# Optimization experiments

Measured on AMD Instinct MI355X. Metric: run time of the kernel, lower is better.

The kernel has to match this reference:

```python
import jax, jax.numpy as jnp
import numpy as np

N = 6144
FEAT = 512
HID = 256
KMAX = 50
KNN = 20
SPATIAL_DECAY = 50.0
THR = 0.1


def setup_inputs() -> dict:
    key = jax.random.key(0)
    ks = jax.random.split(key, 4)
    features = jax.random.normal(ks[0], (N, FEAT), dtype=jnp.float32)
    # spatial coordinates in a ~1000um slide, matches spatial_decay=50
    positions = jax.random.uniform(ks[1], (N, 2), dtype=jnp.float32) * 1000.0
    W1 = jax.random.normal(ks[2], (FEAT, HID), dtype=jnp.float32) * np.float32(1.0 / np.sqrt(FEAT))
    b1 = jnp.zeros((HID,), jnp.float32)
    W2 = jax.random.normal(ks[3], (HID, KMAX), dtype=jnp.float32) * np.float32(1.0 / np.sqrt(HID))
    b2 = jnp.zeros((KMAX,), jnp.float32)
    return {
        "features": features,
        "positions": positions,
        "lambda_weight": jnp.asarray(0.5, jnp.float32),
        "temperature": jnp.asarray(1.0, jnp.float32),
        "spatial_weight": jnp.asarray(1.0, jnp.float32),
        "W1": W1, "b1": b1, "W2": W2, "b2": b2,
    }


def reference(features, positions, lambda_weight, temperature, spatial_weight, W1, b1, W2, b2):
    n = features.shape[0]
    # --- LearnableAdjacency (Eq. 6) ---
    norm = jnp.maximum(jnp.linalg.norm(features, axis=1, keepdims=True), 1e-12)
    fn = features / norm
    sim = fn @ fn.T                                  # [N,N]
    p2 = jnp.sum(positions * positions, axis=1)
    d2 = jnp.maximum(p2[:, None] + p2[None, :] - 2.0 * (positions @ positions.T), 0.0)
    spatial_k = jnp.exp(-d2 / (2.0 * SPATIAL_DECAY ** 2))
    lam = jax.nn.sigmoid(lambda_weight)
    adj = jax.nn.sigmoid((lam * sim + (1.0 - lam) * spatial_k) * temperature)
    # row-wise top-k mask (scatter of ones)
    _, topk_idx = jax.lax.top_k(adj, KNN)
    mask = jnp.zeros_like(adj).at[jnp.arange(n)[:, None], topk_idx].set(1.0)
    adj = adj * mask

    # --- edge_index <=> binary adjacency (threshold 0.1) ---
    A_bin = (adj > THR).astype(adj.dtype)            # edge pattern used by GCN + loss

    # --- DifferentiablePooling: 2-layer GCN over the edge pattern ---
    # PyG GCNConv: add self-loops (diag already 1 -> becomes 2), deg from target (col) sums,
    # edge norm d_r^{-1/2} d_c^{-1/2}, aggregate at target: out = Mn^T (X W) + b
    M = A_bin + jnp.eye(n, dtype=adj.dtype)
    dinv = jax.lax.rsqrt(jnp.sum(M, axis=0))
    Mn = (dinv[:, None] * M) * dinv[None, :]
    h = jax.nn.relu(Mn.T @ (features @ W1) + b1)
    s = Mn.T @ (h @ W2) + b2
    K = max(5, min(KMAX, int(np.ceil(N / 50))))      # static: 50
    S = jax.nn.softmax(s[:, :K], axis=1)             # [N,K]

    # --- spatial loss (Eq. 9), vectorized segment form ---
    # sum over edges (i,j): (S_i . S_j) * ||p_i - p_j||^2  == sum(S * ((A_bin*d2) @ S))
    E = jnp.sum(A_bin)
    We = A_bin * d2
    L_spatial = spatial_weight * jnp.sum(S * (We @ S)) / E

    # --- coarsening (Eq. 8) ---
    X_t = S.T @ features                             # [K,FEAT]
    A_coarse = S.T @ (adj @ S)                       # [K,K]
    A_t = A_coarse * (A_coarse > THR).astype(A_coarse.dtype)
    return (S, X_t, A_t, L_spatial, lam)
```

## Files before the change

### kernel.cpp

```cpp
#include <hip/hip_runtime.h>
#include <hip/hip_bf16.h>
#include <math.h>

#define N_PTS   6144
#define FEAT    512
#define HID     256
#define KMAX    50
#define KNN     20
#define THR     0.1f
#define CW      1536
#define NCHUNK  4

typedef unsigned short u16;
typedef __attribute__((ext_vector_type(8))) short bf16x8;
typedef __attribute__((ext_vector_type(8))) u16   u16x8;
typedef __attribute__((ext_vector_type(4))) float f32x4;

__device__ __forceinline__ u16 f2bf(float x) {
    union { float f; unsigned u; } a; a.f = x;
    unsigned r = (a.u + 0x7fffu + ((a.u >> 16) & 1u)) >> 16;
    return (u16)r;
}
__device__ __forceinline__ float bf2f(u16 h) {
    union { unsigned u; float f; } a; a.u = ((unsigned)h) << 16;
    return a.f;
}

__device__ __forceinline__ void gload16(const void* g, void* l) {
    __builtin_amdgcn_global_load_lds(
        (const __attribute__((address_space(1))) void*)g,
        (__attribute__((address_space(3))) void*)l, 16, 0, 0);
}

__global__ void init_kernel(int* __restrict__ indeg, int* __restrict__ fillc,
                            float* __restrict__ Ac, float* __restrict__ Xt,
                            int* __restrict__ ec) {
    int t = blockIdx.x * blockDim.x + threadIdx.x;
    if (t < N_PTS) { indeg[t] = 0; fillc[t] = 0; }
    if (t < KMAX * KMAX) Ac[t] = 0.f;
    if (t < KMAX * FEAT) Xt[t] = 0.f;
    if (t == 0) { ec[0] = 0; }
}

__global__ __launch_bounds__(64) void normalize_kernel(const float* __restrict__ f,
                                                       u16* __restrict__ fnh,
                                                       u16* __restrict__ fnl,
                                                       u16* __restrict__ fh_,
                                                       u16* __restrict__ fl_) {
    int row = blockIdx.x, lane = threadIdx.x;
    const float4* fr = (const float4*)(f + (size_t)row * FEAT);
    float4 v0 = fr[lane * 2 + 0];
    float4 v1 = fr[lane * 2 + 1];
    float ss = v0.x * v0.x + v0.y * v0.y + v0.z * v0.z + v0.w * v0.w
             + v1.x * v1.x + v1.y * v1.y + v1.z * v1.z + v1.w * v1.w;
#pragma unroll
    for (int m = 1; m < 64; m <<= 1) ss += __shfl_xor(ss, m);
    float nrm = fmaxf(sqrtf(ss), 1e-12f);
    float r[8] = { v0.x, v0.y, v0.z, v0.w, v1.x, v1.y, v1.z, v1.w };
    u16x8 h, l, rh, rl;
#pragma unroll
    for (int q = 0; q < 8; q++) {
        float vn = r[q] / nrm;
        u16 hb = f2bf(vn);
        h[q] = hb; l[q] = f2bf(vn - bf2f(hb));
        u16 rb = f2bf(r[q]);
        rh[q] = rb; rl[q] = f2bf(r[q] - bf2f(rb));
    }
    size_t base = (size_t)row * FEAT + lane * 8;
    *(u16x8*)(fnh + base) = h;
    *(u16x8*)(fnl + base) = l;
    *(u16x8*)(fh_ + base) = rh;
    *(u16x8*)(fl_ + base) = rl;
}

__global__ void p2_kernel(const float* __restrict__ pos, float* __restrict__ p2) {
    int i = blockIdx.x * blockDim.x + threadIdx.x;
    if (i < N_PTS) {
        float x = pos[2 * i], y = pos[2 * i + 1];
        p2[i] = x * x + y * y;
    }
}

__global__ __launch_bounds__(256) void w1t_split_kernel(const float* __restrict__ W1,
                                                        u16* __restrict__ th,
                                                        u16* __restrict__ tl) {
    int n = blockIdx.x;
    for (int k = threadIdx.x; k < FEAT; k += 256) {
        float v = W1[(size_t)k * HID + n];
        u16 hb = f2bf(v);
        th[(size_t)n * FEAT + k] = hb;
        tl[(size_t)n * FEAT + k] = f2bf(v - bf2f(hb));
    }
}

__global__ __launch_bounds__(256) void w2t_split_kernel(const float* __restrict__ W2,
                                                        u16* __restrict__ th,
                                                        u16* __restrict__ tl) {
    int n = blockIdx.x, k = threadIdx.x;
    float v = (n < KMAX) ? W2[(size_t)k * KMAX + n] : 0.f;
    u16 hb = f2bf(v);
    th[(size_t)n * HID + k] = hb;
    tl[(size_t)n * HID + k] = f2bf(v - bf2f(hb));
}


__global__ __launch_bounds__(512) void gemm_adj_mfma_kernel(
    const u16* __restrict__ fnh, const u16* __restrict__ fnl,
    const float* __restrict__ pos, const float* __restrict__ p2,
    const float* __restrict__ lamw, const float* __restrict__ tempw,
    float* __restrict__ out, int c0) {
    __shared__ u16 Ah[128 * 32], Al[128 * 32], Bh[128 * 32], Bl[128 * 32];
    const int tid  = threadIdx.x;
    const int lane = tid & 63, wid = tid >> 6;
    const int wm = wid >> 2, wn = wid & 3;
    const int flat = blockIdx.y * gridDim.x + blockIdx.x;
    const int nwg  = gridDim.x * gridDim.y;
    const int swzb = (flat & 7) * (nwg >> 3) + (flat >> 3);
    const int bx = swzb % gridDim.x, by = swzb / gridDim.x;
    const int bm  = by * 128;
    const int bnl = bx * 128;
    const int bng = c0 + bnl;

    const int sbuf = wid >> 1, shalf = wid & 1;
    const u16* src = (sbuf & 1) ? fnl : fnh;
    u16* dst = (sbuf == 0) ? Ah : (sbuf == 1) ? Al : (sbuf == 2) ? Bh : Bl;
    const int grow = (sbuf >> 1) ? bng : bm;
    const u16* gbase = src + (size_t)(grow + shalf * 64 + (lane >> 2)) * FEAT
                     + (((lane & 3) ^ ((lane >> 3) & 3)) * 8);
    u16* ldst = dst + (shalf * 64) * 32;

    f32x4 acc[4][2];
#pragma unroll
    for (int m = 0; m < 4; m++)
#pragma unroll
        for (int n = 0; n < 2; n++) acc[m][n] = (f32x4){0.f, 0.f, 0.f, 0.f};

    const int fr = lane & 15;
    const int ks = lane >> 4;
    const int ksw = (ks ^ ((fr >> 1) & 3)) * 8;
    const int abase = (wm * 64 + fr) * 32 + ksw;
    const int bbase = (wn * 32 + fr) * 32 + ksw;

    for (int k0 = 0; k0 < FEAT; k0 += 32) {
#pragma unroll
        for (int i = 0; i < 4; i++)
            gload16(gbase + k0 + (size_t)i * 16 * FEAT, ldst + i * 512);
        __syncthreads();
        bf16x8 ahf[4], alf[4], bhf[2], blf[2];
#pragma unroll
        for (int m = 0; m < 4; m++) {
            ahf[m] = *(const bf16x8*)&Ah[abase + m * 16 * 32];
            alf[m] = *(const bf16x8*)&Al[abase + m * 16 * 32];
        }
#pragma unroll
        for (int n = 0; n < 2; n++) {
            bhf[n] = *(const bf16x8*)&Bh[bbase + n * 16 * 32];
            blf[n] = *(const bf16x8*)&Bl[bbase + n * 16 * 32];
        }
#pragma unroll
        for (int m = 0; m < 4; m++)
#pragma unroll
            for (int n = 0; n < 2; n++) {
                acc[m][n] = __builtin_amdgcn_mfma_f32_16x16x32_bf16(ahf[m], bhf[n], acc[m][n], 0, 0, 0);
                acc[m][n] = __builtin_amdgcn_mfma_f32_16x16x32_bf16(ahf[m], blf[n], acc[m][n], 0, 0, 0);
                acc[m][n] = __builtin_amdgcn_mfma_f32_16x16x32_bf16(alf[m], bhf[n], acc[m][n], 0, 0, 0);
            }
        __syncthreads();
    }

    float lam  = 1.f / (1.f + __expf(-lamw[0]));
    float temp = tempw[0];
    float p2c[2], pxc[2], pyc[2];
#pragma unroll
    for (int n = 0; n < 2; n++) {
        int cg = bng + wn * 32 + n * 16 + fr;
        p2c[n] = p2[cg]; pxc[n] = pos[2 * cg]; pyc[n] = pos[2 * cg + 1];
    }
#pragma unroll
    for (int m = 0; m < 4; m++) {
#pragma unroll
        for (int reg = 0; reg < 4; reg++) {
            int rrow = bm + wm * 64 + m * 16 + ks * 4 + reg;
            float p2r = p2[rrow], pxr = pos[2 * rrow], pyr = pos[2 * rrow + 1];
#pragma unroll
            for (int n = 0; n < 2; n++) {
                float sim = acc[m][n][reg];
                float d2 = fmaxf(p2r + p2c[n] - 2.f * (pxr * pxc[n] + pyr * pyc[n]), 0.f);
                float sk = __expf(-d2 * (1.f / 5000.f));
                float arg = (lam * sim + (1.f - lam) * sk) * temp;
                out[(size_t)rrow * CW + bnl + wn * 32 + n * 16 + fr] = 1.f / (1.f + __expf(-arg));
            }
        }
    }
}

__global__ __launch_bounds__(256) void gemm_z_kernel(
    const u16* __restrict__ xh, const u16* __restrict__ xl,
    const u16* __restrict__ w1th, const u16* __restrict__ w1tl,
    float* __restrict__ Z) {
    __shared__ u16 Ah[128 * 32], Al[128 * 32], Bh[128 * 32], Bl[128 * 32];
    const int tid  = threadIdx.x;
    const int lane = tid & 63, wid = tid >> 6;
    const int wm = wid >> 1, wn = wid & 1;
    const int flat = blockIdx.y * gridDim.x + blockIdx.x;
    const int nwg  = gridDim.x * gridDim.y;
    const int swzb = (flat & 7) * (nwg >> 3) + (flat >> 3);
    const int bm = (swzb / gridDim.x) * 128;
    const int bn = (swzb % gridDim.x) * 128;

    const u16* src; u16* dst; int grow;
    if      (wid == 0) { src = xh;   dst = Ah; grow = bm; }
    else if (wid == 1) { src = xl;   dst = Al; grow = bm; }
    else if (wid == 2) { src = w1th; dst = Bh; grow = bn; }
    else               { src = w1tl; dst = Bl; grow = bn; }
    const u16* gbase = src + (size_t)(grow + (lane >> 2)) * FEAT
                     + (((lane & 3) ^ ((lane >> 3) & 3)) * 8);

    f32x4 acc[4][4];
#pragma unroll
    for (int m = 0; m < 4; m++)
#pragma unroll
        for (int n = 0; n < 4; n++) acc[m][n] = (f32x4){0.f, 0.f, 0.f, 0.f};

    const int fr = lane & 15;
    const int ks = lane >> 4;
    const int ksw = (ks ^ ((fr >> 1) & 3)) * 8;
    const int abase = (wm * 64 + fr) * 32 + ksw;
    const int bbase = (wn * 64 + fr) * 32 + ksw;

    for (int k0 = 0; k0 < FEAT; k0 += 32) {
#pragma unroll
        for (int i = 0; i < 8; i++)
            gload16(gbase + k0 + (size_t)i * 16 * FEAT, dst + i * 512);
        __syncthreads();
        bf16x8 ahf[4], alf[4], bhf[4], blf[4];
#pragma unroll
        for (int m = 0; m < 4; m++) {
            ahf[m] = *(const bf16x8*)&Ah[abase + m * 16 * 32];
            alf[m] = *(const bf16x8*)&Al[abase + m * 16 * 32];
        }
#pragma unroll
        for (int n = 0; n < 4; n++) {
            bhf[n] = *(const bf16x8*)&Bh[bbase + n * 16 * 32];
            blf[n] = *(const bf16x8*)&Bl[bbase + n * 16 * 32];
        }
#pragma unroll
        for (int m = 0; m < 4; m++)
#pragma unroll
            for (int n = 0; n < 4; n++) {
                acc[m][n] = __builtin_amdgcn_mfma_f32_16x16x32_bf16(ahf[m], bhf[n], acc[m][n], 0, 0, 0);
                acc[m][n] = __builtin_amdgcn_mfma_f32_16x16x32_bf16(ahf[m], blf[n], acc[m][n], 0, 0, 0);
                acc[m][n] = __builtin_amdgcn_mfma_f32_16x16x32_bf16(alf[m], bhf[n], acc[m][n], 0, 0, 0);
            }
        __syncthreads();
    }
#pragma unroll
    for (int m = 0; m < 4; m++)
#pragma unroll
        for (int reg = 0; reg < 4; reg++) {
            int rrow = bm + wm * 64 + m * 16 + ks * 4 + reg;
#pragma unroll
            for (int n = 0; n < 4; n++)
                Z[(size_t)rrow * HID + bn + wn * 64 + n * 16 + fr] = acc[m][n][reg];
        }
}

__global__ __launch_bounds__(256) void gemm_y_kernel(
    const u16* __restrict__ hh, const u16* __restrict__ hl,
    const u16* __restrict__ w2th, const u16* __restrict__ w2tl,
    float* __restrict__ Y) {
    __shared__ u16 Ah[128 * 32], Al[128 * 32], Bh[64 * 32], Bl[64 * 32];
    const int tid  = threadIdx.x;
    const int lane = tid & 63, wid = tid >> 6;
    const int wm = wid >> 1, wn = wid & 1;
    const int bm = blockIdx.x * 128;

    const u16* src; u16* dst; int grow; int nld;
    if      (wid == 0) { src = hh;   dst = Ah; grow = bm; nld = 8; }
    else if (wid == 1) { src = hl;   dst = Al; grow = bm; nld = 8; }
    else if (wid == 2) { src = w2th; dst = Bh; grow = 0;  nld = 4; }
    else               { src = w2tl; dst = Bl; grow = 0;  nld = 4; }
    const u16* gbase = src + (size_t)(grow + (lane >> 2)) * HID
                     + (((lane & 3) ^ ((lane >> 3) & 3)) * 8);

    f32x4 acc[4][2];
#pragma unroll
    for (int m = 0; m < 4; m++)
#pragma unroll
        for (int n = 0; n < 2; n++) acc[m][n] = (f32x4){0.f, 0.f, 0.f, 0.f};

    const int fr = lane & 15;
    const int ks = lane >> 4;
    const int ksw = (ks ^ ((fr >> 1) & 3)) * 8;
    const int abase = (wm * 64 + fr) * 32 + ksw;
    const int bbase = (wn * 32 + fr) * 32 + ksw;

    for (int k0 = 0; k0 < HID; k0 += 32) {
        for (int i = 0; i < nld; i++)
            gload16(gbase + k0 + (size_t)i * 16 * HID, dst + i * 512);
        __syncthreads();
        bf16x8 ahf[4], alf[4], bhf[2], blf[2];
#pragma unroll
        for (int m = 0; m < 4; m++) {
            ahf[m] = *(const bf16x8*)&Ah[abase + m * 16 * 32];
            alf[m] = *(const bf16x8*)&Al[abase + m * 16 * 32];
        }
#pragma unroll
        for (int n = 0; n < 2; n++) {
            bhf[n] = *(const bf16x8*)&Bh[bbase + n * 16 * 32];
            blf[n] = *(const bf16x8*)&Bl[bbase + n * 16 * 32];
        }
#pragma unroll
        for (int m = 0; m < 4; m++)
#pragma unroll
            for (int n = 0; n < 2; n++) {
                acc[m][n] = __builtin_amdgcn_mfma_f32_16x16x32_bf16(ahf[m], bhf[n], acc[m][n], 0, 0, 0);
                acc[m][n] = __builtin_amdgcn_mfma_f32_16x16x32_bf16(ahf[m], blf[n], acc[m][n], 0, 0, 0);
                acc[m][n] = __builtin_amdgcn_mfma_f32_16x16x32_bf16(alf[m], bhf[n], acc[m][n], 0, 0, 0);
            }
        __syncthreads();
    }
#pragma unroll
    for (int m = 0; m < 4; m++)
#pragma unroll
        for (int reg = 0; reg < 4; reg++) {
            int rrow = bm + wm * 64 + m * 16 + ks * 4 + reg;
#pragma unroll
            for (int n = 0; n < 2; n++) {
                int col = wn * 32 + n * 16 + fr;
                if (col < KMAX) Y[(size_t)rrow * KMAX + col] = acc[m][n][reg];
            }
        }
}

__global__ __launch_bounds__(256) void topk_kernel(const float* __restrict__ chunk,
                                                   float* __restrict__ gval,
                                                   int* __restrict__ gidx, int c0) {
    const int lane = threadIdx.x & 63;
    const int row  = blockIdx.x * 4 + (threadIdx.x >> 6);
    float lv = -INFINITY; int li = -1;
    if (c0 > 0 && lane < KNN) {
        lv = gval[(size_t)row * KNN + lane];
        li = gidx[(size_t)row * KNN + lane];
    }
    float T = __shfl(lv, KNN - 1);
    const float4* rp = (const float4*)(chunk + (size_t)row * CW);
    float4 q[CW / 256];
#pragma unroll
    for (int b = 0; b < CW / 256; b++) q[b] = rp[lane + 64 * b];
#pragma unroll
    for (int b = 0; b < CW / 256; b++) {
        float vv[4] = { q[b].x, q[b].y, q[b].z, q[b].w };
        float bm4 = fmaxf(fmaxf(vv[0], vv[1]), fmaxf(vv[2], vv[3]));
#pragma unroll
        for (int msk = 1; msk < 64; msk <<= 1) bm4 = fmaxf(bm4, __shfl_xor(bm4, msk));
        if (bm4 <= T) continue;
#pragma unroll
        for (int e = 0; e < 4; e++) {
            unsigned long long bal = __ballot(vv[e] > T);
            while (bal) {
                int src = __ffsll((unsigned long long)bal) - 1;
                bal &= bal - 1;
                float cv = __shfl(vv[e], src);
                if (cv > T) {
                    int cc = c0 + 4 * (src + 64 * b) + e;
                    float up = __shfl_up(lv, 1);
                    int  upi = __shfl_up(li, 1);
                    if (lane == 0) up = INFINITY;
                    bool keep = lv > cv;
                    float nv = keep ? lv : (up > cv ? cv : up);
                    int  ni = keep ? li : (up > cv ? cc : upi);
                    lv = nv; li = ni;
                    T = __shfl(lv, KNN - 1);
                }
            }
        }
    }
    if (lane < KNN) {
        gval[(size_t)row * KNN + lane] = lv;
        gidx[(size_t)row * KNN + lane] = li;
    }
}

__global__ void degree_kernel(const float* __restrict__ gval, const int* __restrict__ gidx,
                              int* __restrict__ indeg, int* __restrict__ ec) {
    int e = blockIdx.x * blockDim.x + threadIdx.x;
    bool pass = gval[e] > THR;
    if (pass) atomicAdd(&indeg[gidx[e]], 1);
    unsigned long long b = __ballot(pass);
    if ((threadIdx.x & 63) == 0) atomicAdd(ec, (int)__popcll(b));
}

__global__ __launch_bounds__(1024) void scan_kernel(const int* __restrict__ indeg,
                                                    int* __restrict__ offs,
                                                    float* __restrict__ dinv) {
    __shared__ int part[1024];
    int tid = threadIdx.x;
    int d[6], loc[6], s = 0;
#pragma unroll
    for (int q = 0; q < 6; q++) { d[q] = indeg[tid * 6 + q]; loc[q] = s; s += d[q]; }
    part[tid] = s;
    __syncthreads();
    for (int off = 1; off < 1024; off <<= 1) {
        int v = (tid >= off) ? part[tid - off] : 0;
        __syncthreads();
        part[tid] += v;
        __syncthreads();
    }
    int pre = (tid > 0) ? part[tid - 1] : 0;
#pragma unroll
    for (int q = 0; q < 6; q++) {
        offs[tid * 6 + q] = pre + loc[q];
        dinv[tid * 6 + q] = 1.0f / sqrtf((float)(d[q] + 1));
    }
    if (tid == 1023) offs[N_PTS] = part[1023];
}

__global__ void fill_kernel(const float* __restrict__ gval, const int* __restrict__ gidx,
                            const int* __restrict__ offs, int* __restrict__ fillc,
                            int* __restrict__ csc) {
    int e = blockIdx.x * blockDim.x + threadIdx.x;
    if (gval[e] > THR) {
        int j = gidx[e];
        int pos = offs[j] + atomicAdd(&fillc[j], 1);
        csc[pos] = e / KNN;
    }
}

__global__ __launch_bounds__(256) void agg1_kernel(const float* __restrict__ Z,
                                                   const int* __restrict__ offs,
                                                   const int* __restrict__ csc,
                                                   const float* __restrict__ dinv,
                                                   const float* __restrict__ b1,
                                                   u16* __restrict__ hh,
                                                   u16* __restrict__ hl) {
    int j = blockIdx.x, f = threadIdx.x;
    float dj = dinv[j];
    float acc = dj * Z[(size_t)j * HID + f];
    int e = offs[j], e1 = offs[j + 1];
    for (; e + 4 <= e1; e += 4) {
        int i0 = csc[e], i1 = csc[e + 1], i2 = csc[e + 2], i3 = csc[e + 3];
        float w0 = dinv[i0], w1 = dinv[i1], w2 = dinv[i2], w3 = dinv[i3];
        float z0 = Z[(size_t)i0 * HID + f], z1 = Z[(size_t)i1 * HID + f];
        float z2 = Z[(size_t)i2 * HID + f], z3 = Z[(size_t)i3 * HID + f];
        acc = fmaf(w0, z0, acc); acc = fmaf(w1, z1, acc);
        acc = fmaf(w2, z2, acc); acc = fmaf(w3, z3, acc);
    }
    for (; e < e1; e++) {
        int i = csc[e];
        acc = fmaf(dinv[i], Z[(size_t)i * HID + f], acc);
    }
    float hv = fmaxf(acc * dj + b1[f], 0.f);
    u16 hb = f2bf(hv);
    hh[(size_t)j * HID + f] = hb;
    hl[(size_t)j * HID + f] = f2bf(hv - bf2f(hb));
}

__global__ __launch_bounds__(256) void agg2_softmax_kernel(const float* __restrict__ Y,
                                                           const int* __restrict__ offs,
                                                           const int* __restrict__ csc,
                                                           const float* __restrict__ dinv,
                                                           const float* __restrict__ b2,
                                                           float* __restrict__ S) {
    int c = threadIdx.x & 63;
    int j = blockIdx.x * 4 + (threadIdx.x >> 6);
    bool act = c < KMAX;
    float dj = dinv[j];
    float acc = act ? dj * Y[(size_t)j * KMAX + c] : 0.f;
    int e = offs[j], e1 = offs[j + 1];
    for (; e + 4 <= e1; e += 4) {
        int i0 = csc[e], i1 = csc[e + 1], i2 = csc[e + 2], i3 = csc[e + 3];
        float w0 = dinv[i0], w1 = dinv[i1], w2 = dinv[i2], w3 = dinv[i3];
        float y0 = act ? Y[(size_t)i0 * KMAX + c] : 0.f;
        float y1 = act ? Y[(size_t)i1 * KMAX + c] : 0.f;
        float y2 = act ? Y[(size_t)i2 * KMAX + c] : 0.f;
        float y3 = act ? Y[(size_t)i3 * KMAX + c] : 0.f;
        acc = fmaf(w0, y0, acc); acc = fmaf(w1, y1, acc);
        acc = fmaf(w2, y2, acc); acc = fmaf(w3, y3, acc);
    }
    for (; e < e1; e++) {
        int i = csc[e];
        if (act) acc = fmaf(dinv[i], Y[(size_t)i * KMAX + c], acc);
    }
    float s = act ? (acc * dj + b2[c]) : -INFINITY;
    float m = s;
#pragma unroll
    for (int msk = 1; msk < 64; msk <<= 1) m = fmaxf(m, __shfl_xor(m, msk));
    float ex = act ? expf(s - m) : 0.f;
    float tot = ex;
#pragma unroll
    for (int msk = 1; msk < 64; msk <<= 1) tot += __shfl_xor(tot, msk);
    if (act) S[(size_t)j * KMAX + c] = ex / tot;
}

__global__ __launch_bounds__(256) void rowops_kernel(const float* __restrict__ S,
                                                     const int* __restrict__ gidx,
                                                     const float* __restrict__ gval,
                                                     const float* __restrict__ pos,
                                                     const float* __restrict__ p2,
                                                     float* __restrict__ AS,
                                                     float* __restrict__ lossrow) {
    const int lane = threadIdx.x & 63;
    const int i = blockIdx.x * 4 + (threadIdx.x >> 6);
    const int c = lane;
    const bool act = c < KMAX;
    int jl = 0; float vl = 0.f, d2l = 0.f;
    if (lane < KNN) {
        jl = gidx[(size_t)i * KNN + lane];
        vl = gval[(size_t)i * KNN + lane];
        float pxi = pos[2 * i], pyi = pos[2 * i + 1], p2i = p2[i];
        d2l = fmaxf(p2i + p2[jl] - 2.f * (pxi * pos[2 * jl] + pyi * pos[2 * jl + 1]), 0.f);
    }
    float asum = 0.f, wsum = 0.f;
#pragma unroll
    for (int e = 0; e < KNN; e++) {
        int j = __shfl(jl, e);
        float v = __shfl(vl, e);
        float d2 = __shfl(d2l, e);
        float sv = act ? S[(size_t)j * KMAX + c] : 0.f;
        asum = fmaf(v, sv, asum);
        if (v > THR) wsum = fmaf(d2, sv, wsum);
    }
    if (act) AS[(size_t)i * KMAX + c] = asum;
    float li = act ? S[(size_t)i * KMAX + c] * wsum : 0.f;
#pragma unroll
    for (int m = 1; m < 64; m <<= 1) li += __shfl_xor(li, m);
    if (lane == 0) lossrow[i] = li;
}

__global__ __launch_bounds__(1024) void loss_reduce_kernel(const float* __restrict__ lossrow,
                                                           float* __restrict__ lossb) {
    int tid = threadIdx.x;
    float s = 0.f;
#pragma unroll
    for (int q = 0; q < 6; q++) s += lossrow[tid + 1024 * q];
#pragma unroll
    for (int m = 1; m < 64; m <<= 1) s += __shfl_xor(s, m);
    __shared__ float ws[16];
    if ((tid & 63) == 0) ws[tid >> 6] = s;
    __syncthreads();
    if (tid == 0) {
        float t = 0.f;
#pragma unroll
        for (int q = 0; q < 16; q++) t += ws[q];
        lossb[0] = t;
    }
}

__global__ __launch_bounds__(256) void coarseA_kernel(const float* __restrict__ S,
                                                      const float* __restrict__ AS,
                                                      float* __restrict__ Ac) {
    __shared__ float Ss[16][50];
    __shared__ float Bs[16][50];
    int tid = threadIdx.x;
    int n0 = blockIdx.x * 128;
    float acc[10];
    int ca[10], cb[10];
#pragma unroll
    for (int q = 0; q < 10; q++) {
        acc[q] = 0.f;
        int cell = tid + 256 * q;
        ca[q] = cell / 50; cb[q] = cell % 50;
    }
    for (int sub = 0; sub < 8; sub++) {
        int base = n0 + sub * 16;
        for (int idx = tid; idx < 16 * 50; idx += 256) {
            int r = idx / 50, c = idx % 50;
            Ss[r][c] = S[(size_t)(base + r) * KMAX + c];
            Bs[r][c] = AS[(size_t)(base + r) * KMAX + c];
        }
        __syncthreads();
        for (int r = 0; r < 16; r++) {
#pragma unroll
            for (int q = 0; q < 10; q++) {
                if (tid + 256 * q < 2500)
                    acc[q] = fmaf(Ss[r][ca[q]], Bs[r][cb[q]], acc[q]);
            }
        }
        __syncthreads();
    }
#pragma unroll
    for (int q = 0; q < 10; q++) {
        int cell = tid + 256 * q;
        if (cell < 2500) atomicAdd(&Ac[cell], acc[q]);
    }
}

__global__ __launch_bounds__(128) void coarseX_kernel(const float* __restrict__ S,
                                                      const float* __restrict__ X,
                                                      float* __restrict__ Xt) {
    __shared__ float Ss[16][50];
    int tid = threadIdx.x;
    int f = (blockIdx.x & 3) * 128 + tid;
    int n0 = (blockIdx.x >> 2) * 128;
    float acc[50];
#pragma unroll
    for (int a = 0; a < 50; a++) acc[a] = 0.f;
    for (int sub = 0; sub < 8; sub++) {
        int base = n0 + sub * 16;
        for (int idx = tid; idx < 16 * 50; idx += 128) {
            int r = idx / 50, c = idx % 50;
            Ss[r][c] = S[(size_t)(base + r) * KMAX + c];
        }
        __syncthreads();
        for (int r = 0; r < 16; r++) {
            float xv = X[(size_t)(base + r) * FEAT + f];
#pragma unroll
            for (int a = 0; a < 50; a++) acc[a] = fmaf(Ss[r][a], xv, acc[a]);
        }
        __syncthreads();
    }
#pragma unroll
    for (int a = 0; a < 50; a++) atomicAdd(&Xt[(size_t)a * FEAT + f], acc[a]);
}

__global__ void finalize_kernel(const float* __restrict__ Ac, const float* __restrict__ loss,
                                const int* __restrict__ ec, const float* __restrict__ sw,
                                const float* __restrict__ lamw, float* __restrict__ out_At,
                                float* __restrict__ out_scalars) {
    int t = blockIdx.x * blockDim.x + threadIdx.x;
    if (t < KMAX * KMAX) {
        float v = Ac[t];
        out_At[t] = (v > THR) ? v : 0.f;
    }
    if (t == 0) {
        out_scalars[0] = sw[0] * loss[0] / (float)ec[0];
        out_scalars[1] = 1.f / (1.f + expf(-lamw[0]));
    }
}

extern "C" void kernel_launch(void* const* d_in, const int* in_sizes, int n_in,
                              void* d_out, int out_size, void* d_ws, size_t ws_size,
                              hipStream_t stream) {
    const float* features = (const float*)d_in[0];
    const float* positions = (const float*)d_in[1];
    const float* lambda_w  = (const float*)d_in[2];
    const float* temp_w    = (const float*)d_in[3];
    const float* spatial_w = (const float*)d_in[4];
    const float* W1 = (const float*)d_in[5];
    const float* b1 = (const float*)d_in[6];
    const float* W2 = (const float*)d_in[7];
    const float* b2 = (const float*)d_in[8];

    float* out = (float*)d_out;
    float* out_S  = out;
    float* out_Xt = out + (size_t)N_PTS * KMAX;
    float* out_At = out_Xt + KMAX * FEAT;
    float* out_sc = out_At + KMAX * KMAX;

    char* ws = (char*)d_ws;
    size_t off = 0;
    auto alloc = [&](size_t bytes) { size_t o = off; off = (off + bytes + 255) & ~(size_t)255; return o; };
    u16*   fnh     = (u16*)  (ws + alloc((size_t)N_PTS * FEAT * 2));
    u16*   fnl     = (u16*)  (ws + alloc((size_t)N_PTS * FEAT * 2));
    u16*   fh      = (u16*)  (ws + alloc((size_t)N_PTS * FEAT * 2));
    u16*   fl      = (u16*)  (ws + alloc((size_t)N_PTS * FEAT * 2));
    float* p2      = (float*)(ws + alloc((size_t)N_PTS * 4));
    float* adjchnk = (float*)(ws + alloc((size_t)N_PTS * CW * 4));
    float* gval    = (float*)(ws + alloc((size_t)N_PTS * KNN * 4));
    int*   gidx    = (int*)  (ws + alloc((size_t)N_PTS * KNN * 4));
    int*   indeg   = (int*)  (ws + alloc((size_t)N_PTS * 4));
    int*   fillc   = (int*)  (ws + alloc((size_t)N_PTS * 4));
    int*   offs    = (int*)  (ws + alloc((size_t)(N_PTS + 1) * 4));
    float* dinv    = (float*)(ws + alloc((size_t)N_PTS * 4));
    int*   csc     = (int*)  (ws + alloc((size_t)N_PTS * KNN * 4));
    u16*   w1th    = (u16*)  (ws + alloc((size_t)HID * FEAT * 2));
    u16*   w1tl    = (u16*)  (ws + alloc((size_t)HID * FEAT * 2));
    u16*   w2th    = (u16*)  (ws + alloc((size_t)64 * HID * 2));
    u16*   w2tl    = (u16*)  (ws + alloc((size_t)64 * HID * 2));
    float* lossrow = (float*)(ws + alloc((size_t)N_PTS * 4));
    float* Ac      = (float*)(ws + alloc((size_t)KMAX * KMAX * 4));
    float* lossb   = (float*)(ws + alloc(4));
    int*   ecnt    = (int*)  (ws + alloc(4));

    char* ov = (char*)adjchnk;
    float* Z  = (float*)(ov);
    u16*   hh = (u16*)  (ov + 7 * 1024 * 1024);
    u16*   hl = (u16*)  (ov + 11 * 1024 * 1024);
    float* Y  = (float*)(ov + 15 * 1024 * 1024);
    float* AS = (float*)(ov + 17 * 1024 * 1024);

    init_kernel<<<(KMAX * FEAT + 255) / 256, 256, 0, stream>>>(indeg, fillc, Ac, out_Xt, ecnt);
    normalize_kernel<<<N_PTS, 64, 0, stream>>>(features, fnh, fnl, fh, fl);
    p2_kernel<<<(N_PTS + 255) / 256, 256, 0, stream>>>(positions, p2);
    w1t_split_kernel<<<HID, 256, 0, stream>>>(W1, w1th, w1tl);
    w2t_split_kernel<<<64, 256, 0, stream>>>(W2, w2th, w2tl);
    for (int c = 0; c < NCHUNK; c++) {
        gemm_adj_mfma_kernel<<<dim3(CW / 128, N_PTS / 128), 512, 0, stream>>>(
            fnh, fnl, positions, p2, lambda_w, temp_w, adjchnk, c * CW);
        topk_kernel<<<N_PTS / 4, 256, 0, stream>>>(adjchnk, gval, gidx, c * CW);
    }
    degree_kernel<<<(N_PTS * KNN) / 256, 256, 0, stream>>>(gval, gidx, indeg, ecnt);
    scan_kernel<<<1, 1024, 0, stream>>>(indeg, offs, dinv);
    fill_kernel<<<(N_PTS * KNN) / 256, 256, 0, stream>>>(gval, gidx, offs, fillc, csc);
    gemm_z_kernel<<<dim3(HID / 128, N_PTS / 128), 256, 0, stream>>>(fh, fl, w1th, w1tl, Z);
    agg1_kernel<<<N_PTS, HID, 0, stream>>>(Z, offs, csc, dinv, b1, hh, hl);
    gemm_y_kernel<<<N_PTS / 128, 256, 0, stream>>>(hh, hl, w2th, w2tl, Y);
    agg2_softmax_kernel<<<N_PTS / 4, 256, 0, stream>>>(Y, offs, csc, dinv, b2, out_S);
    rowops_kernel<<<N_PTS / 4, 256, 0, stream>>>(out_S, gidx, gval, positions, p2, AS, lossrow);
    loss_reduce_kernel<<<1, 1024, 0, stream>>>(lossrow, lossb);
    coarseA_kernel<<<N_PTS / 128, 256, 0, stream>>>(out_S, AS, Ac);
    coarseX_kernel<<<(N_PTS / 128) * 4, 128, 0, stream>>>(out_S, features, out_Xt);
    finalize_kernel<<<(KMAX * KMAX + 255) / 256, 256, 0, stream>>>(Ac, lossb, ecnt, spatial_w, lambda_w, out_At, out_sc);
}
```

Before: 520.5 us.

## Replace atomic coarsening accumulation with per-chunk partials and deterministic reductions

The coarse A and X products now split the node dimension into 96 chunks of 64 rows. Each block writes its partial product to scratch space instead of atomically adding into the outputs, and a separate reduction kernel (plus the finalize kernel for A) sums the partials. This removes global float atomics and the zero-init of the outputs, and raises block count for coarseX to 768 single-wave blocks. The cost is an extra kernel launch and roughly 10 MB of partial-sum traffic written and then read back.

```diff
diff --git a/kernel.cpp b/kernel.cpp
--- a/kernel.cpp
+++ b/kernel.cpp
@@ -10,6 +10,8 @@
 #define THR     0.1f
 #define CW      1536
 #define NCHUNK  4
+#define CXC     64
+#define NCHX    (N_PTS / CXC)
 
 typedef unsigned short u16;
 typedef __attribute__((ext_vector_type(8))) short bf16x8;
@@ -33,12 +35,9 @@
 }
 
 __global__ void init_kernel(int* __restrict__ indeg, int* __restrict__ fillc,
-                            float* __restrict__ Ac, float* __restrict__ Xt,
                             int* __restrict__ ec) {
     int t = blockIdx.x * blockDim.x + threadIdx.x;
     if (t < N_PTS) { indeg[t] = 0; fillc[t] = 0; }
-    if (t < KMAX * KMAX) Ac[t] = 0.f;
-    if (t < KMAX * FEAT) Xt[t] = 0.f;
     if (t == 0) { ec[0] = 0; }
 }
 
@@ -549,11 +548,18 @@
 
 __global__ __launch_bounds__(256) void coarseA_kernel(const float* __restrict__ S,
                                                       const float* __restrict__ AS,
-                                                      float* __restrict__ Ac) {
-    __shared__ float Ss[16][50];
-    __shared__ float Bs[16][50];
+                                                      float* __restrict__ Acp) {
+    __shared__ float Ss[CXC][50];
+    __shared__ float Bs[CXC][50];
     int tid = threadIdx.x;
-    int n0 = blockIdx.x * 128;
+    int ch = blockIdx.x;
+    int i0 = ch * CXC;
+    for (int idx = tid; idx < CXC * 50; idx += 256) {
+        int r = idx / 50, c = idx % 50;
+        Ss[r][c] = S[(size_t)(i0 + r) * KMAX + c];
+        Bs[r][c] = AS[(size_t)(i0 + r) * KMAX + c];
+    }
+    __syncthreads();
     float acc[10];
     int ca[10], cb[10];
 #pragma unroll
@@ -562,65 +568,79 @@
         int cell = tid + 256 * q;
         ca[q] = cell / 50; cb[q] = cell % 50;
     }
-    for (int sub = 0; sub < 8; sub++) {
-        int base = n0 + sub * 16;
-        for (int idx = tid; idx < 16 * 50; idx += 256) {
-            int r = idx / 50, c = idx % 50;
-            Ss[r][c] = S[(size_t)(base + r) * KMAX + c];
-            Bs[r][c] = AS[(size_t)(base + r) * KMAX + c];
-        }
-        __syncthreads();
-        for (int r = 0; r < 16; r++) {
-#pragma unroll
-            for (int q = 0; q < 10; q++) {
-                if (tid + 256 * q < 2500)
-                    acc[q] = fmaf(Ss[r][ca[q]], Bs[r][cb[q]], acc[q]);
-            }
-        }
-        __syncthreads();
+    for (int r = 0; r < CXC; r++) {
+#pragma unroll
+        for (int q = 0; q < 10; q++) {
+            if (tid + 256 * q < 2500)
+                acc[q] = fmaf(Ss[r][ca[q]], Bs[r][cb[q]], acc[q]);
+        }
     }
 #pragma unroll
     for (int q = 0; q < 10; q++) {
         int cell = tid + 256 * q;
-        if (cell < 2500) atomicAdd(&Ac[cell], acc[q]);
-    }
-}
-
-__global__ __launch_bounds__(128) void coarseX_kernel(const float* __restrict__ S,
-                                                      const float* __restrict__ X,
+        if (cell < 2500) Acp[(size_t)ch * 2500 + cell] = acc[q];
+    }
+}
+
+__global__ __launch_bounds__(64) void coarseX_kernel(const float* __restrict__ S,
+                                                     const float* __restrict__ X,
+                                                     float* __restrict__ Xtp) {
+    __shared__ float Ss[CXC][50];
+    const int lane = threadIdx.x;
+    const int ch = blockIdx.x >> 3;
+    const int f = ((blockIdx.x & 7) << 6) + lane;
+    const int i0 = ch * CXC;
+    for (int idx = lane; idx < CXC * 50; idx += 64) {
+        Ss[idx / 50][idx % 50] = S[(size_t)(i0 + idx / 50) * KMAX + idx % 50];
+    }
+    __syncthreads();
+    float acc[50];
+#pragma unroll
+    for (int a = 0; a < 50; a++) acc[a] = 0.f;
+    const float* xp = X + (size_t)i0 * FEAT + f;
+#pragma unroll 4
+    for (int r = 0; r < CXC; r++) {
+        float xv = xp[(size_t)r * FEAT];
+#pragma unroll
+        for (int a = 0; a < 50; a++) acc[a] = fmaf(Ss[r][a], xv, acc[a]);
+    }
+#pragma unroll
+    for (int a = 0; a < 50; a++)
+        Xtp[((size_t)ch * KMAX + a) * FEAT + f] = acc[a];
+}
+
+__global__ __launch_bounds__(256) void reduceX_kernel(const float* __restrict__ Xtp,
                                                       float* __restrict__ Xt) {
-    __shared__ float Ss[16][50];
-    int tid = threadIdx.x;
-    int f = (blockIdx.x & 3) * 128 + tid;
-    int n0 = (blockIdx.x >> 2) * 128;
-    float acc[50];
-#pragma unroll
-    for (int a = 0; a < 50; a++) acc[a] = 0.f;
-    for (int sub = 0; sub < 8; sub++) {
-        int base = n0 + sub * 16;
-        for (int idx = tid; idx < 16 * 50; idx += 128) {
-            int r = idx / 50, c = idx % 50;
-            Ss[r][c] = S[(size_t)(base + r) * KMAX + c];
-        }
-        __syncthreads();
-        for (int r = 0; r < 16; r++) {
-            float xv = X[(size_t)(base + r) * FEAT + f];
-#pragma unroll
-            for (int a = 0; a < 50; a++) acc[a] = fmaf(Ss[r][a], xv, acc[a]);
-        }
-        __syncthreads();
-    }
-#pragma unroll
-    for (int a = 0; a < 50; a++) atomicAdd(&Xt[(size_t)a * FEAT + f], acc[a]);
-}
-
-__global__ void finalize_kernel(const float* __restrict__ Ac, const float* __restrict__ loss,
-                                const int* __restrict__ ec, const float* __restrict__ sw,
-                                const float* __restrict__ lamw, float* __restrict__ out_At,
-                                float* __restrict__ out_scalars) {
+    int cell = blockIdx.x * 256 + threadIdx.x;
+    if (cell < KMAX * FEAT) {
+        float s0 = 0.f, s1 = 0.f, s2 = 0.f, s3 = 0.f;
+        for (int ch = 0; ch < NCHX; ch += 4) {
+            s0 += Xtp[(size_t)ch * KMAX * FEAT + cell];
+            s1 += Xtp[(size_t)(ch + 1) * KMAX * FEAT + cell];
+            s2 += Xtp[(size_t)(ch + 2) * KMAX * FEAT + cell];
+            s3 += Xtp[(size_t)(ch + 3) * KMAX * FEAT + cell];
+        }
+        Xt[cell] = (s0 + s1) + (s2 + s3);
+    }
+}
+
+__global__ __launch_bounds__(256) void finalize_kernel(const float* __restrict__ Acp,
+                                                       const float* __restrict__ loss,
+                                                       const int* __restrict__ ec,
+                                                       const float* __restrict__ sw,
+                                                       const float* __restrict__ lamw,
+                                                       float* __restrict__ out_At,
+                                                       float* __restrict__ out_scalars) {
     int t = blockIdx.x * blockDim.x + threadIdx.x;
     if (t < KMAX * KMAX) {
-        float v = Ac[t];
+        float s0 = 0.f, s1 = 0.f, s2 = 0.f, s3 = 0.f;
+        for (int ch = 0; ch < NCHX; ch += 4) {
+            s0 += Acp[(size_t)ch * 2500 + t];
+            s1 += Acp[(size_t)(ch + 1) * 2500 + t];
+            s2 += Acp[(size_t)(ch + 2) * 2500 + t];
+            s3 += Acp[(size_t)(ch + 3) * 2500 + t];
+        }
+        float v = (s0 + s1) + (s2 + s3);
         out_At[t] = (v > THR) ? v : 0.f;
     }
     if (t == 0) {
@@ -669,18 +689,19 @@
     u16*   w2th    = (u16*)  (ws + alloc((size_t)64 * HID * 2));
     u16*   w2tl    = (u16*)  (ws + alloc((size_t)64 * HID * 2));
     float* lossrow = (float*)(ws + alloc((size_t)N_PTS * 4));
-    float* Ac      = (float*)(ws + alloc((size_t)KMAX * KMAX * 4));
     float* lossb   = (float*)(ws + alloc(4));
     int*   ecnt    = (int*)  (ws + alloc(4));
 
     char* ov = (char*)adjchnk;
-    float* Z  = (float*)(ov);
-    u16*   hh = (u16*)  (ov + 7 * 1024 * 1024);
-    u16*   hl = (u16*)  (ov + 11 * 1024 * 1024);
-    float* Y  = (float*)(ov + 15 * 1024 * 1024);
-    float* AS = (float*)(ov + 17 * 1024 * 1024);
-
-    init_kernel<<<(KMAX * FEAT + 255) / 256, 256, 0, stream>>>(indeg, fillc, Ac, out_Xt, ecnt);
+    float* Z   = (float*)(ov);
+    u16*   hh  = (u16*)  (ov + 7 * 1024 * 1024);
+    u16*   hl  = (u16*)  (ov + 11 * 1024 * 1024);
+    float* Y   = (float*)(ov + 15 * 1024 * 1024);
+    float* AS  = (float*)(ov + 17 * 1024 * 1024);
+    float* Xtp = (float*)(ov + 19 * 1024 * 1024);
+    float* Acp = (float*)(ov + 30 * 1024 * 1024);
+
+    init_kernel<<<(N_PTS + 255) / 256, 256, 0, stream>>>(indeg, fillc, ecnt);
     normalize_kernel<<<N_PTS, 64, 0, stream>>>(features, fnh, fnl, fh, fl);
     p2_kernel<<<(N_PTS + 255) / 256, 256, 0, stream>>>(positions, p2);
     w1t_split_kernel<<<HID, 256, 0, stream>>>(W1, w1th, w1tl);
@@ -699,7 +720,8 @@
     agg2_softmax_kernel<<<N_PTS / 4, 256, 0, stream>>>(Y, offs, csc, dinv, b2, out_S);
     rowops_kernel<<<N_PTS / 4, 256, 0, stream>>>(out_S, gidx, gval, positions, p2, AS, lossrow);
     loss_reduce_kernel<<<1, 1024, 0, stream>>>(lossrow, lossb);
-    coarseA_kernel<<<N_PTS / 128, 256, 0, stream>>>(out_S, AS, Ac);
-    coarseX_kernel<<<(N_PTS / 128) * 4, 128, 0, stream>>>(out_S, features, out_Xt);
-    finalize_kernel<<<(KMAX * KMAX + 255) / 256, 256, 0, stream>>>(Ac, lossb, ecnt, spatial_w, lambda_w, out_At, out_sc);
-}
+    coarseA_kernel<<<NCHX, 256, 0, stream>>>(out_S, AS, Acp);
+    coarseX_kernel<<<NCHX * 8, 64, 0, stream>>>(out_S, features, Xtp);
+    reduceX_kernel<<<(KMAX * FEAT + 255) / 256, 256, 0, stream>>>(Xtp, out_Xt);
+    finalize_kernel<<<(KMAX * KMAX + 255) / 256, 256, 0, stream>>>(Acp, lossb, ecnt, spatial_w, lambda_w, out_At, out_sc);
+}
```

Measured after the change: 493.9 us. -5.1%, faster.
